# Optimization experiments

Hardware: AMD Instinct MI355X
Metric: run time of the kernel (lower is better)

## Reference

```python
import jax, jax.numpy as jnp
import numpy as np

B, S, DIM = 2, 4096, 768
G = DIM // 3          # gate_dim = 256
H, DK = 4, G // 4     # heads=4, d_k=64
SCALE = 1.0 / np.sqrt(DK)


def setup_inputs() -> dict:
    key = jax.random.key(0)
    ks = jax.random.split(key, 9)
    r = lambda k, shp, s: (jax.random.normal(k, shp, dtype=jnp.float32) * s)
    w_s = 1.0 / np.sqrt(G)
    return {
        "x": r(ks[0], (B, S, DIM), 1.0),
        "wq": r(ks[1], (G, G), w_s), "bq": r(ks[2], (G,), 0.01),
        "wk": r(ks[3], (G, G), w_s), "bk": r(ks[4], (G,), 0.01),
        "wv": r(ks[5], (G, G), w_s), "bv": r(ks[6], (G,), 0.01),
        "wo": r(ks[7], (G, G), w_s), "bo": r(ks[8], (G,), 0.01),
    }


def reference(x, wq, bq, wk, bk, wv, bv, wo, bo):
    # chunk(3, dim=-1): q/k/v slices of width G
    xq, xk, xv = x[..., :G], x[..., G:2 * G], x[..., 2 * G:3 * G]
    # linear projections then split into heads: [b, s, h, d]
    q = (xq @ wq.T + bq).reshape(B, S, H, DK)
    k = (xk @ wk.T + bk).reshape(B, S, H, DK)
    v = (xv @ wv.T + bv).reshape(B, S, H, DK)
    scores = jnp.einsum('bihd,bjhd->bijh', q, k) * SCALE  # [b, i, j, h]
    # NOTE: original applies Softmax(dim=1) -> over the QUERY axis i
    attn = jax.nn.softmax(scores, axis=1)
    out = jnp.einsum('bijh,bjhd->bihd', attn, v).reshape(B, S, G)
    return out @ wo.T + bo
```

## Files before the change

kernel.cpp:

```cpp
#include <hip/hip_runtime.h>

#define SEQ   4096
#define HH    4
#define SCALE 0.125f

typedef __bf16 bf16x8 __attribute__((ext_vector_type(8)));
typedef __bf16 bf16x4 __attribute__((ext_vector_type(4)));
typedef float  f32x4  __attribute__((ext_vector_type(4)));

constexpr size_t OFF_W16  = 0;
constexpr size_t OFF_A    = 131072;
constexpr size_t OFF_PZ   = 163840;
constexpr size_t OFF_AO   = 294912;
constexpr size_t OFF_X16  = 9732096;
constexpr size_t OFF_Q16  = 12877824;
constexpr size_t K16OFF   = 2097152;
constexpr size_t V16OFF   = 4194304;

__device__ __forceinline__ f32x4 mf(bf16x8 a, bf16x8 b, f32x4 c) {
    return __builtin_amdgcn_mfma_f32_16x16x32_bf16(a, b, c, 0, 0, 0);
}

__device__ __forceinline__ void gload16(const __bf16* g, __bf16* l) {
    __builtin_amdgcn_global_load_lds(
        (const __attribute__((address_space(1))) unsigned int*)g,
        (__attribute__((address_space(3))) unsigned int*)l, 16, 0, 0);
}

__global__ void k_prep(const float* __restrict__ x,
                       const float* __restrict__ wq, const float* __restrict__ wk,
                       const float* __restrict__ wv, const float* __restrict__ wo,
                       float* __restrict__ ws) {
    int bx = blockIdx.x, t = threadIdx.x;
    if (bx < 6144) {
        size_t i4 = ((size_t)bx * 256 + t) * 4;
        float4 v = *(const float4*)(x + i4);
        bf16x4 o = {(__bf16)v.x, (__bf16)v.y, (__bf16)v.z, (__bf16)v.w};
        *(bf16x4*)((__bf16*)(ws + OFF_X16) + i4) = o;
    } else if (bx < 6400) {
        int q = bx - 6144;
        int y = q >> 6;
        const float* src = (y == 0) ? wq : (y == 1) ? wk : (y == 2) ? wv : wo;
        size_t i4 = ((size_t)(q & 63) * 256 + t) * 4;
        float4 v = *(const float4*)(src + i4);
        bf16x4 o = {(__bf16)v.x, (__bf16)v.y, (__bf16)v.z, (__bf16)v.w};
        *(bf16x4*)((__bf16*)(ws + OFF_W16) + (size_t)y * 65536 + i4) = o;
    } else {
        size_t i4 = ((size_t)(bx - 6400) * 256 + t) * 4;
        *(float4*)(ws + OFF_AO + i4) = make_float4(0.f, 0.f, 0.f, 0.f);
    }
}

__global__ __launch_bounds__(256) void k_qkv_mfma(const float* __restrict__ bq,
                                                  const float* __restrict__ bk,
                                                  const float* __restrict__ bv,
                                                  float* __restrict__ ws) {
    int t = threadIdx.x, lane = t & 63, w = t >> 6;
    int yw = blockIdx.y;
    int row0 = blockIdx.x * 64 + w * 16;
    int mrow = lane & 15, quad = lane >> 4;
    const __bf16* X16 = (const __bf16*)(ws + OFF_X16);
    const __bf16* W16 = (const __bf16*)(ws + OFF_W16) + (size_t)yw * 65536;
    const float* bias = (yw == 0) ? bq : (yw == 1) ? bk : bv;
    __bf16* Qb = (__bf16*)(ws + OFF_Q16);
    f32x4 acc[16];
#pragma unroll
    for (int n = 0; n < 16; n++) acc[n] = {0.f, 0.f, 0.f, 0.f};
    const __bf16* ap = X16 + (size_t)(row0 + mrow) * 768 + yw * 256 + quad * 8;
    const __bf16* bp = W16 + (size_t)mrow * 256 + quad * 8;
    for (int kc = 0; kc < 256; kc += 32) {
        bf16x8 a = *(const bf16x8*)(ap + kc);
#pragma unroll
        for (int nt = 0; nt < 16; nt++) {
            bf16x8 b = *(const bf16x8*)(bp + (size_t)nt * 16 * 256 + kc);
            acc[nt] = mf(a, b, acc[nt]);
        }
    }
#pragma unroll
    for (int nt = 0; nt < 16; nt++) {
        int n = nt * 16 + mrow;
        float bb = bias[n];
        int h = n >> 6, d = n & 63;
#pragma unroll
        for (int r = 0; r < 4; r++) {
            int sg = row0 + quad * 4 + r;
            int b_ = sg >> 12, s = sg & 4095;
            int bh = b_ * HH + h;
            float val = acc[nt][r] + bb;
            if (yw <= 1) {
                int tile = s >> 4, m = s & 15, frag = d >> 5, q2 = (d >> 3) & 3, e = d & 7;
                size_t idx = (((size_t)bh * 256 + tile) * 2 + frag) * 512 +
                             (size_t)(q2 * 16 + m) * 8 + e;
                ((yw == 0) ? Qb : Qb + K16OFF)[idx] = (__bf16)val;
            } else {
                int jc = s >> 5, qk = (s >> 3) & 3, e = s & 7;
                int nd = d >> 4, nl = d & 15;
                size_t idx = (((size_t)bh * 128 + jc) * 4 + nd) * 512 +
                             (size_t)(qk * 16 + nl) * 8 + e;
                Qb[V16OFF + idx] = (__bf16)val;
            }
        }
    }
}

__global__ __launch_bounds__(256) void k_colstats(float* __restrict__ ws) {
    __shared__ __bf16 qbuf[2][4096];
    int t = threadIdx.x, lane = t & 63, w = t >> 6;
    int jb = blockIdx.x, iy = blockIdx.y, bh = blockIdx.z;
    int jt0 = jb * 8 + w * 2;
    const __bf16* Qp = (const __bf16*)(ws + OFF_Q16);
    const __bf16* Kp = Qp + K16OFF;
    const __bf16* kb = Kp + (((size_t)bh * 256 + jt0) * 2) * 512 + lane * 8;
    bf16x8 bk00 = *(const bf16x8*)(kb);
    bf16x8 bk01 = *(const bf16x8*)(kb + 512);
    bf16x8 bk10 = *(const bf16x8*)(kb + 1024);
    bf16x8 bk11 = *(const bf16x8*)(kb + 1536);
    const __bf16* q0 = Qp + (((size_t)bh * 256 + iy * 64) * 2) * 512 +
                       w * 1024 + lane * 8;
    gload16(q0, qbuf[0] + w * 1024);
    gload16(q0 + 512, qbuf[0] + w * 1024 + 512);
    __syncthreads();
    float z0 = 0.f, z1 = 0.f;
    for (int ic = 0; ic < 16; ic++) {
        const __bf16* cur = qbuf[ic & 1];
        if (ic < 15) {
            const __bf16* qn = Qp + (((size_t)bh * 256 + iy * 64 + (ic + 1) * 4) * 2) * 512 +
                               w * 1024 + lane * 8;
            gload16(qn, qbuf[(ic + 1) & 1] + w * 1024);
            gload16(qn + 512, qbuf[(ic + 1) & 1] + w * 1024 + 512);
        }
#pragma unroll
        for (int it = 0; it < 4; it++) {
            bf16x8 a0 = *(const bf16x8*)(cur + it * 1024 + lane * 8);
            bf16x8 a1 = *(const bf16x8*)(cur + it * 1024 + 512 + lane * 8);
            f32x4 c0 = {0.f, 0.f, 0.f, 0.f};
            c0 = mf(a0, bk00, c0);
            c0 = mf(a1, bk01, c0);
            f32x4 c1 = {0.f, 0.f, 0.f, 0.f};
            c1 = mf(a0, bk10, c1);
            c1 = mf(a1, bk11, c1);
#pragma unroll
            for (int r = 0; r < 4; r++) {
                z0 += __expf(fmaf(c0[r], SCALE, -16.0f));
                z1 += __expf(fmaf(c1[r], SCALE, -16.0f));
            }
        }
        __syncthreads();
    }
    z0 += __shfl_xor(z0, 16, 64);
    z0 += __shfl_xor(z0, 32, 64);
    z1 += __shfl_xor(z1, 16, 64);
    z1 += __shfl_xor(z1, 32, 64);
    if (lane < 16) {
        size_t o = OFF_PZ + (size_t)iy * 32768 + (size_t)bh * SEQ + jt0 * 16 + lane;
        ws[o] = z0;
        ws[o + 16] = z1;
    }
}

__global__ void k_afin(float* __restrict__ ws) {
    int idx = blockIdx.x * 256 + threadIdx.x;
    const float* pz = ws + OFF_PZ;
    float Z = pz[idx] + pz[32768 + (size_t)idx] + pz[65536 + (size_t)idx] +
              pz[98304 + (size_t)idx];
    ws[OFF_A + idx] = -16.0f - __logf(Z);
}

__global__ __launch_bounds__(256) void k_attnpv(float* __restrict__ ws) {
    __shared__ __bf16 ldsK[2][2048], ldsV[2][2048], ptile[4 * 1280];
    int t = threadIdx.x, lane = t & 63, w = t >> 6;
    int jy = blockIdx.y, bh = blockIdx.z;
    int it0 = blockIdx.x * 8 + w * 2;
    int mrow = lane & 15, quad = lane >> 4;
    const __bf16* Qp = (const __bf16*)(ws + OFF_Q16);
    const __bf16* Kp = Qp + K16OFF;
    const __bf16* Vp = Qp + V16OFF;
    const float* Ac = ws + OFF_A + (size_t)bh * SEQ;
    __bf16* pt = ptile + w * 1280;

    const __bf16* qb = Qp + (((size_t)bh * 256 + it0) * 2) * 512 + lane * 8;
    bf16x8 aq00 = *(const bf16x8*)(qb);
    bf16x8 aq01 = *(const bf16x8*)(qb + 512);
    bf16x8 aq10 = *(const bf16x8*)(qb + 1024);
    bf16x8 aq11 = *(const bf16x8*)(qb + 1536);

    f32x4 oacc[2][4];
#pragma unroll
    for (int tt = 0; tt < 2; tt++)
#pragma unroll
        for (int nd = 0; nd < 4; nd++) oacc[tt][nd] = {0.f, 0.f, 0.f, 0.f};

    int jbase = jy * 1024;
    {
        const __bf16* kg = Kp + (((size_t)bh * 256 + (jbase >> 4)) * 2) * 512 +
                           w * 512 + lane * 8;
        gload16(kg, ldsK[0] + w * 512);
        const __bf16* vg = Vp + (((size_t)bh * 128 + (jbase >> 5)) * 4) * 512 +
                           w * 512 + lane * 8;
        gload16(vg, ldsV[0] + w * 512);
    }
    __syncthreads();

    for (int jt = 0; jt < 32; jt++) {
        int j0 = jbase + jt * 32;
        const __bf16* curK = ldsK[jt & 1];
        const __bf16* curV = ldsV[jt & 1];
        if (jt < 31) {
            int jn = j0 + 32;
            const __bf16* kg = Kp + (((size_t)bh * 256 + (jn >> 4)) * 2) * 512 +
                               w * 512 + lane * 8;
            gload16(kg, ldsK[(jt + 1) & 1] + w * 512);
            const __bf16* vg = Vp + (((size_t)bh * 128 + (jn >> 5)) * 4) * 512 +
                               w * 512 + lane * 8;
            gload16(vg, ldsV[(jt + 1) & 1] + w * 512);
        }
        float ca0 = Ac[j0 + mrow], ca1 = Ac[j0 + 16 + mrow];
        bf16x8 ck0 = *(const bf16x8*)(curK + lane * 8);
        bf16x8 ck1 = *(const bf16x8*)(curK + 512 + lane * 8);
        bf16x8 ck2 = *(const bf16x8*)(curK + 1024 + lane * 8);
        bf16x8 ck3 = *(const bf16x8*)(curK + 1536 + lane * 8);
#pragma unroll
        for (int tt = 0; tt < 2; tt++) {
            bf16x8 a0 = tt ? aq10 : aq00;
            bf16x8 a1 = tt ? aq11 : aq01;
            f32x4 c0 = {0.f, 0.f, 0.f, 0.f};
            c0 = mf(a0, ck0, c0);
            c0 = mf(a1, ck1, c0);
            f32x4 c1 = {0.f, 0.f, 0.f, 0.f};
            c1 = mf(a0, ck2, c1);
            c1 = mf(a1, ck3, c1);
#pragma unroll
            for (int r = 0; r < 4; r++) {
                float p0 = __expf(fmaf(c0[r], SCALE, ca0));
                pt[(tt * 16 + quad * 4 + r) * 40 + mrow] = (__bf16)p0;
                float p1 = __expf(fmaf(c1[r], SCALE, ca1));
                pt[(tt * 16 + quad * 4 + r) * 40 + 16 + mrow] = (__bf16)p1;
            }
        }
        bf16x8 ap0 = *(const bf16x8*)(pt + mrow * 40 + quad * 8);
        bf16x8 ap1 = *(const bf16x8*)(pt + (16 + mrow) * 40 + quad * 8);
#pragma unroll
        for (int nd = 0; nd < 4; nd++) {
            bf16x8 bv = *(const bf16x8*)(curV + nd * 512 + lane * 8);
            oacc[0][nd] = mf(ap0, bv, oacc[0][nd]);
            oacc[1][nd] = mf(ap1, bv, oacc[1][nd]);
        }
        __syncthreads();
    }

    int b = bh >> 2, h = bh & 3;
    float* AO = ws + OFF_AO;
#pragma unroll
    for (int tt = 0; tt < 2; tt++) {
#pragma unroll
        for (int nd = 0; nd < 4; nd++) {
#pragma unroll
            for (int r = 0; r < 4; r++) {
                int i = (it0 + tt) * 16 + quad * 4 + r;
                int d = nd * 16 + mrow;
                atomicAdd(&AO[((size_t)(b * SEQ + i)) * 256 + h * 64 + d],
                          oacc[tt][nd][r]);
            }
        }
    }
}

__global__ __launch_bounds__(256) void k_outproj_mfma(const float* __restrict__ bo,
                                                      float* __restrict__ ws,
                                                      float* __restrict__ out) {
    int t = threadIdx.x, lane = t & 63, w = t >> 6;
    int row0 = blockIdx.x * 64 + w * 16;
    int mrow = lane & 15, quad = lane >> 4;
    const float* AO = ws + OFF_AO;
    const __bf16* W16 = (const __bf16*)(ws + OFF_W16) + (size_t)3 * 65536;
    f32x4 acc[16];
#pragma unroll
    for (int n = 0; n < 16; n++) acc[n] = {0.f, 0.f, 0.f, 0.f};
    const float* ap = AO + (size_t)(row0 + mrow) * 256 + quad * 8;
    const __bf16* bp = W16 + (size_t)mrow * 256 + quad * 8;
    for (int kc = 0; kc < 256; kc += 32) {
        float4 u = *(const float4*)(ap + kc);
        float4 v = *(const float4*)(ap + kc + 4);
        bf16x8 a = {(__bf16)u.x, (__bf16)u.y, (__bf16)u.z, (__bf16)u.w,
                    (__bf16)v.x, (__bf16)v.y, (__bf16)v.z, (__bf16)v.w};
#pragma unroll
        for (int nt = 0; nt < 16; nt++) {
            bf16x8 b = *(const bf16x8*)(bp + (size_t)nt * 16 * 256 + kc);
            acc[nt] = mf(a, b, acc[nt]);
        }
    }
#pragma unroll
    for (int nt = 0; nt < 16; nt++) {
        int n = nt * 16 + mrow;
        float bb = bo[n];
#pragma unroll
        for (int r = 0; r < 4; r++) {
            int sg = row0 + quad * 4 + r;
            out[(size_t)sg * 256 + n] = acc[nt][r] + bb;
        }
    }
}

extern "C" void kernel_launch(void* const* d_in, const int* in_sizes, int n_in,
                              void* d_out, int out_size, void* d_ws, size_t ws_size,
                              hipStream_t stream) {
    const float* x  = (const float*)d_in[0];
    const float* wq = (const float*)d_in[1];
    const float* bq = (const float*)d_in[2];
    const float* wk = (const float*)d_in[3];
    const float* bk = (const float*)d_in[4];
    const float* wv = (const float*)d_in[5];
    const float* bv = (const float*)d_in[6];
    const float* wo = (const float*)d_in[7];
    const float* bo = (const float*)d_in[8];
    float* ws = (float*)d_ws;
    float* out = (float*)d_out;

    k_prep<<<8448, 256, 0, stream>>>(x, wq, wk, wv, wo, ws);
    k_qkv_mfma<<<dim3(128, 3), 256, 0, stream>>>(bq, bk, bv, ws);
    k_colstats<<<dim3(32, 4, 8), 256, 0, stream>>>(ws);
    k_afin<<<128, 256, 0, stream>>>(ws);
    k_attnpv<<<dim3(32, 4, 8), 256, 0, stream>>>(ws);
    k_outproj_mfma<<<128, 256, 0, stream>>>(bo, ws, out);
}
```

Measured before the change: 247.1 us.

## Keep P in registers via transposed scores and 16x16x16 MFMA for PV

The attention kernel computes the transposed score tile (K as the A operand, Q as B), so each lane's accumulator output directly forms a 4-element bf16 B-fragment for a 16x16x16 bf16 MFMA. The per-wave LDS P tile round trip is gone. The V tensor is re-laid out in the projection kernel into 16-row chunks matching the new fragment shape, and the atomic output indexing is transposed to match. This trades the LDS write/read and sync for twice as many smaller MFMA instructions on the PV product.

```diff
diff --git a/kernel.cpp b/kernel.cpp
--- a/kernel.cpp
+++ b/kernel.cpp
@@ -6,6 +6,7 @@
 
 typedef __bf16 bf16x8 __attribute__((ext_vector_type(8)));
 typedef __bf16 bf16x4 __attribute__((ext_vector_type(4)));
+typedef short  s16x4  __attribute__((ext_vector_type(4)));
 typedef float  f32x4  __attribute__((ext_vector_type(4)));
 
 constexpr size_t OFF_W16  = 0;
@@ -19,6 +20,19 @@
 
 __device__ __forceinline__ f32x4 mf(bf16x8 a, bf16x8 b, f32x4 c) {
     return __builtin_amdgcn_mfma_f32_16x16x32_bf16(a, b, c, 0, 0, 0);
+}
+
+__device__ __forceinline__ f32x4 mf16(bf16x4 a, bf16x4 b, f32x4 c) {
+#if __has_builtin(__builtin_amdgcn_mfma_f32_16x16x16bf16_1k)
+    s16x4 as = __builtin_bit_cast(s16x4, a);
+    s16x4 bs = __builtin_bit_cast(s16x4, b);
+    return __builtin_amdgcn_mfma_f32_16x16x16bf16_1k(as, bs, c, 0, 0, 0);
+#else
+    f32x4 d = c;
+    asm volatile("v_mfma_f32_16x16x16_bf16 %0, %1, %2, %0"
+                 : "+v"(d) : "v"(a), "v"(b));
+    return d;
+#endif
 }
 
 __device__ __forceinline__ void gload16(const __bf16* g, __bf16* l) {
@@ -93,10 +107,10 @@
                              (size_t)(q2 * 16 + m) * 8 + e;
                 ((yw == 0) ? Qb : Qb + K16OFF)[idx] = (__bf16)val;
             } else {
-                int jc = s >> 5, qk = (s >> 3) & 3, e = s & 7;
-                int nd = d >> 4, nl = d & 15;
-                size_t idx = (((size_t)bh * 128 + jc) * 4 + nd) * 512 +
-                             (size_t)(qk * 16 + nl) * 8 + e;
+                int jc = s >> 4, q = (s >> 2) & 3, e = s & 3;
+                int nd = d >> 4, dl = d & 15;
+                size_t idx = (((size_t)bh * 256 + jc) * 4 + nd) * 256 +
+                             (size_t)(q * 16 + dl) * 4 + e;
                 Qb[V16OFF + idx] = (__bf16)val;
             }
         }
@@ -167,7 +181,7 @@
 }
 
 __global__ __launch_bounds__(256) void k_attnpv(float* __restrict__ ws) {
-    __shared__ __bf16 ldsK[2][2048], ldsV[2][2048], ptile[4 * 1280];
+    __shared__ __bf16 ldsK[2][2048], ldsV[2][2048];
     int t = threadIdx.x, lane = t & 63, w = t >> 6;
     int jy = blockIdx.y, bh = blockIdx.z;
     int it0 = blockIdx.x * 8 + w * 2;
@@ -176,13 +190,13 @@
     const __bf16* Kp = Qp + K16OFF;
     const __bf16* Vp = Qp + V16OFF;
     const float* Ac = ws + OFF_A + (size_t)bh * SEQ;
-    __bf16* pt = ptile + w * 1280;
 
     const __bf16* qb = Qp + (((size_t)bh * 256 + it0) * 2) * 512 + lane * 8;
-    bf16x8 aq00 = *(const bf16x8*)(qb);
-    bf16x8 aq01 = *(const bf16x8*)(qb + 512);
-    bf16x8 aq10 = *(const bf16x8*)(qb + 1024);
-    bf16x8 aq11 = *(const bf16x8*)(qb + 1536);
+    bf16x8 qf[2][2];
+    qf[0][0] = *(const bf16x8*)(qb);
+    qf[0][1] = *(const bf16x8*)(qb + 512);
+    qf[1][0] = *(const bf16x8*)(qb + 1024);
+    qf[1][1] = *(const bf16x8*)(qb + 1536);
 
     f32x4 oacc[2][4];
 #pragma unroll
@@ -195,7 +209,7 @@
         const __bf16* kg = Kp + (((size_t)bh * 256 + (jbase >> 4)) * 2) * 512 +
                            w * 512 + lane * 8;
         gload16(kg, ldsK[0] + w * 512);
-        const __bf16* vg = Vp + (((size_t)bh * 128 + (jbase >> 5)) * 4) * 512 +
+        const __bf16* vg = Vp + ((size_t)bh * 256 + (jbase >> 4)) * 1024 +
                            w * 512 + lane * 8;
         gload16(vg, ldsV[0] + w * 512);
     }
@@ -210,40 +224,33 @@
             const __bf16* kg = Kp + (((size_t)bh * 256 + (jn >> 4)) * 2) * 512 +
                                w * 512 + lane * 8;
             gload16(kg, ldsK[(jt + 1) & 1] + w * 512);
-            const __bf16* vg = Vp + (((size_t)bh * 128 + (jn >> 5)) * 4) * 512 +
+            const __bf16* vg = Vp + ((size_t)bh * 256 + (jn >> 4)) * 1024 +
                                w * 512 + lane * 8;
             gload16(vg, ldsV[(jt + 1) & 1] + w * 512);
         }
-        float ca0 = Ac[j0 + mrow], ca1 = Ac[j0 + 16 + mrow];
-        bf16x8 ck0 = *(const bf16x8*)(curK + lane * 8);
-        bf16x8 ck1 = *(const bf16x8*)(curK + 512 + lane * 8);
-        bf16x8 ck2 = *(const bf16x8*)(curK + 1024 + lane * 8);
-        bf16x8 ck3 = *(const bf16x8*)(curK + 1536 + lane * 8);
-#pragma unroll
-        for (int tt = 0; tt < 2; tt++) {
-            bf16x8 a0 = tt ? aq10 : aq00;
-            bf16x8 a1 = tt ? aq11 : aq01;
-            f32x4 c0 = {0.f, 0.f, 0.f, 0.f};
-            c0 = mf(a0, ck0, c0);
-            c0 = mf(a1, ck1, c0);
-            f32x4 c1 = {0.f, 0.f, 0.f, 0.f};
-            c1 = mf(a0, ck2, c1);
-            c1 = mf(a1, ck3, c1);
-#pragma unroll
-            for (int r = 0; r < 4; r++) {
-                float p0 = __expf(fmaf(c0[r], SCALE, ca0));
-                pt[(tt * 16 + quad * 4 + r) * 40 + mrow] = (__bf16)p0;
-                float p1 = __expf(fmaf(c1[r], SCALE, ca1));
-                pt[(tt * 16 + quad * 4 + r) * 40 + 16 + mrow] = (__bf16)p1;
+#pragma unroll
+        for (int jj = 0; jj < 2; jj++) {
+            bf16x8 k0 = *(const bf16x8*)(curK + (jj * 2) * 512 + lane * 8);
+            bf16x8 k1 = *(const bf16x8*)(curK + (jj * 2 + 1) * 512 + lane * 8);
+            bf16x4 vf[4];
+#pragma unroll
+            for (int nd = 0; nd < 4; nd++)
+                vf[nd] = *(const bf16x4*)(curV + (jj * 4 + nd) * 256 + lane * 4);
+            float4 af = *(const float4*)(Ac + j0 + jj * 16 + quad * 4);
+#pragma unroll
+            for (int tt = 0; tt < 2; tt++) {
+                f32x4 c = {0.f, 0.f, 0.f, 0.f};
+                c = mf(k0, qf[tt][0], c);
+                c = mf(k1, qf[tt][1], c);
+                bf16x4 pf;
+                pf[0] = (__bf16)__expf(fmaf(c[0], SCALE, af.x));
+                pf[1] = (__bf16)__expf(fmaf(c[1], SCALE, af.y));
+                pf[2] = (__bf16)__expf(fmaf(c[2], SCALE, af.z));
+                pf[3] = (__bf16)__expf(fmaf(c[3], SCALE, af.w));
+#pragma unroll
+                for (int nd = 0; nd < 4; nd++)
+                    oacc[tt][nd] = mf16(vf[nd], pf, oacc[tt][nd]);
             }
-        }
-        bf16x8 ap0 = *(const bf16x8*)(pt + mrow * 40 + quad * 8);
-        bf16x8 ap1 = *(const bf16x8*)(pt + (16 + mrow) * 40 + quad * 8);
-#pragma unroll
-        for (int nd = 0; nd < 4; nd++) {
-            bf16x8 bv = *(const bf16x8*)(curV + nd * 512 + lane * 8);
-            oacc[0][nd] = mf(ap0, bv, oacc[0][nd]);
-            oacc[1][nd] = mf(ap1, bv, oacc[1][nd]);
         }
         __syncthreads();
     }
@@ -252,12 +259,12 @@
     float* AO = ws + OFF_AO;
 #pragma unroll
     for (int tt = 0; tt < 2; tt++) {
+        int i = (it0 + tt) * 16 + mrow;
 #pragma unroll
         for (int nd = 0; nd < 4; nd++) {
 #pragma unroll
             for (int r = 0; r < 4; r++) {
-                int i = (it0 + tt) * 16 + quad * 4 + r;
-                int d = nd * 16 + mrow;
+                int d = nd * 16 + quad * 4 + r;
                 atomicAdd(&AO[((size_t)(b * SEQ + i)) * 256 + h * 64 + d],
                           oacc[tt][nd][r]);
             }
```

Result: slower. 315.5 us (+27.7%).
